# Performance work log

Measured on AMD Instinct MI355X. Metric: run time of the kernel, lower is better.

The kernel has to match this reference:

```python
import jax, jax.numpy as jnp
import numpy as np

EMBED_DIM = 1024
NUM_HEADS = 16
HEAD_DIM = EMBED_DIM // NUM_HEADS


def setup_inputs() -> dict:
    key = jax.random.key(0)
    ks = jax.random.split(key, 10)
    B, S, D = 4, 2048, EMBED_DIM
    s = 1.0 / np.sqrt(D)
    return {
        "x": jax.random.normal(ks[0], (B, S, D), dtype=jnp.float32),
        "Wq": jax.random.normal(ks[1], (D, D), dtype=jnp.float32) * s,
        "bq": jnp.zeros((D,), dtype=jnp.float32),
        "Wk": jax.random.normal(ks[2], (D, D), dtype=jnp.float32) * s,
        "bk": jnp.zeros((D,), dtype=jnp.float32),
        "Wv": jax.random.normal(ks[3], (D, D), dtype=jnp.float32) * s,
        "bv": jnp.zeros((D,), dtype=jnp.float32),
        "Wo": jax.random.normal(ks[4], (D, D), dtype=jnp.float32) * s,
        "bo": jnp.zeros((D,), dtype=jnp.float32),
        "ln_w": jnp.ones((D,), dtype=jnp.float32),
        "ln_b": jnp.zeros((D,), dtype=jnp.float32),
    }


def _layernorm(x, w, b, eps=1e-5):
    mu = jnp.mean(x, axis=-1, keepdims=True)
    var = jnp.mean(jnp.square(x - mu), axis=-1, keepdims=True)
    return (x - mu) * jax.lax.rsqrt(var + eps) * w + b


def reference(x, Wq, bq, Wk, bk, Wv, bv, Wo, bo, ln_w, ln_b):
    B, S, D = x.shape
    H, hd = NUM_HEADS, HEAD_DIM
    # projections (torch Linear: x @ W.T + b)
    q = (x @ Wq.T + bq).reshape(B, S, H, hd).transpose(0, 2, 1, 3)  # [B,H,S,hd]
    k = (x @ Wk.T + bk).reshape(B, S, H, hd).transpose(0, 2, 1, 3)
    v = (x @ Wv.T + bv).reshape(B, S, H, hd).transpose(0, 2, 1, 3)
    scores = jnp.einsum("bhqd,bhkd->bhqk", q, k) / np.sqrt(hd)
    attn = jax.nn.softmax(scores, axis=-1)
    out = jnp.einsum("bhqk,bhkd->bhqd", attn, v)
    out = out.transpose(0, 2, 1, 3).reshape(B, S, D)
    out = out @ Wo.T + bo
    return _layernorm(out, ln_w, ln_b)
```

## Files before the change

kernel.cpp:

```cpp
#include <hip/hip_runtime.h>
#include <hip/hip_bf16.h>
#include <math.h>

typedef unsigned short u16;
typedef unsigned int   u32;
typedef short bf16x8 __attribute__((ext_vector_type(8)));
typedef float f32x4  __attribute__((ext_vector_type(4)));
typedef float f32x16 __attribute__((ext_vector_type(16)));
typedef u32   u32x4  __attribute__((ext_vector_type(4)));

#define B_   4
#define S_   2048
#define D_   1024
#define H_   16
#define HD_  64
#define M_   (B_*S_)

static __device__ __forceinline__ u16 f2bf(float f) {
  __hip_bfloat16 h = __float2bfloat16(f);
  return *reinterpret_cast<u16*>(&h);
}
static __device__ __forceinline__ u32 pack_bf(float lo, float hi) {
  return (u32)f2bf(lo) | ((u32)f2bf(hi) << 16);
}
static __device__ __forceinline__ u32 pack_bf_trunc(float lo, float hi) {
  return __builtin_amdgcn_perm(__float_as_uint(hi), __float_as_uint(lo), 0x07060302u);
}
static __device__ __forceinline__ f32x16 zero16() {
  f32x16 z;
#pragma unroll
  for (int i = 0; i < 16; ++i) z[i] = 0.f;
  return z;
}

typedef __attribute__((address_space(1))) const u32* gas_t;
typedef __attribute__((address_space(3))) u32* las_t;
static __device__ __forceinline__ void g2l16(const void* g, void* l) {
  __builtin_amdgcn_global_load_lds((gas_t)g, (las_t)l, 16, 0, 0);
}

__global__ __launch_bounds__(256) void cast_all(const float* __restrict__ x,
                                                const float* __restrict__ Wq,
                                                const float* __restrict__ Wk,
                                                const float* __restrict__ Wv,
                                                const float* __restrict__ Wo,
                                                u16* __restrict__ xb,
                                                u16* __restrict__ Wqb,
                                                u16* __restrict__ Wkb,
                                                u16* __restrict__ Wvb,
                                                u16* __restrict__ Wob) {
  int bid = blockIdx.x;
  const float* src;
  u16* dst;
  int off;
  if (bid < 8192) {
    src = x; dst = xb; off = bid;
  } else {
    int t = bid - 8192;
    int w = t >> 10;
    off   = t & 1023;
    src = w == 0 ? Wq : w == 1 ? Wk : w == 2 ? Wv : Wo;
    dst = w == 0 ? Wqb : w == 1 ? Wkb : w == 2 ? Wvb : Wob;
  }
  int i = (off * 256 + threadIdx.x) * 4;
  float4 v = *reinterpret_cast<const float4*>(src + i);
  uint2 o;
  o.x = pack_bf(v.x, v.y);
  o.y = pack_bf(v.z, v.w);
  *reinterpret_cast<uint2*>(dst + i) = o;
}

__global__ __launch_bounds__(256) void gemm_qkv(const u16* __restrict__ A,
                                                const u16* __restrict__ Wq,
                                                const u16* __restrict__ Wk,
                                                const u16* __restrict__ Wv,
                                                const float* __restrict__ bq,
                                                const float* __restrict__ bk,
                                                const float* __restrict__ bv,
                                                u16* __restrict__ Qo,
                                                u16* __restrict__ Ko,
                                                u16* __restrict__ Vo) {
  const int tid  = threadIdx.x;
  const int lane = tid & 63;
  const int wave = tid >> 6;
  const int m16  = lane & 15;
  const int quad = lane >> 4;
  const int wm   = wave & 1;
  const int wn   = wave >> 1;
  const int which = blockIdx.x % 3;
  const int m0   = (blockIdx.x / 3) * 128;
  const int n0   = blockIdx.y * 128;

  const u16* W = which == 0 ? Wq : which == 1 ? Wk : Wv;
  const float* bias = which == 0 ? bq : which == 1 ? bk : bv;

  __shared__ __align__(16) u16 As[128 * 32];
  __shared__ __align__(16) u16 Bs[128 * 32];

  f32x4 acc[4][4];
#pragma unroll
  for (int i = 0; i < 4; ++i)
#pragma unroll
    for (int j = 0; j < 4; ++j) acc[i][j] = (f32x4){0.f, 0.f, 0.f, 0.f};

  for (int k0 = 0; k0 < 1024; k0 += 32) {
#pragma unroll
    for (int i = 0; i < 2; ++i) {
      int e0  = i * 256 + (wave << 6);
      int e   = e0 + lane;
      int row = e >> 2;
      int c8  = (e & 3) * 8;
      g2l16(&A[(size_t)(m0 + row) * 1024 + k0 + c8], &As[e0 * 8]);
      g2l16(&W[(size_t)(n0 + row) * 1024 + k0 + c8], &Bs[e0 * 8]);
    }
    __syncthreads();

    bf16x8 af[4], bfr[4];
#pragma unroll
    for (int mt = 0; mt < 4; ++mt)
      af[mt] = *reinterpret_cast<const bf16x8*>(&As[(wm * 64 + mt * 16 + m16) * 32 + quad * 8]);
#pragma unroll
    for (int nt = 0; nt < 4; ++nt)
      bfr[nt] = *reinterpret_cast<const bf16x8*>(&Bs[(wn * 64 + nt * 16 + m16) * 32 + quad * 8]);

#pragma unroll
    for (int mt = 0; mt < 4; ++mt)
#pragma unroll
      for (int nt = 0; nt < 4; ++nt)
        acc[mt][nt] = __builtin_amdgcn_mfma_f32_16x16x32_bf16(af[mt], bfr[nt], acc[mt][nt], 0, 0, 0);
    __syncthreads();
  }

  const float scale = which == 0 ? 0.125f * 1.44269504f : 1.0f;
  u16* ob = which == 0 ? Qo : which == 1 ? Ko : Vo;
#pragma unroll
  for (int mt = 0; mt < 4; ++mt) {
#pragma unroll
    for (int nt = 0; nt < 4; ++nt) {
      int col = n0 + wn * 64 + nt * 16 + m16;
      float bi = bias[col];
      int row0 = m0 + wm * 64 + mt * 16 + quad * 4;
      int b = row0 >> 11, s = row0 & 2047;
      int h = col >> 6,  d = col & 63;
      float v[4];
#pragma unroll
      for (int r = 0; r < 4; ++r) v[r] = (acc[mt][nt][r] + bi) * scale;
      if (which < 2) {
#pragma unroll
        for (int r = 0; r < 4; ++r)
          ob[(size_t)((b * H_ + h) * S_ + s + r) * HD_ + d] = f2bf(v[r]);
      } else {
        uint2 w;
        w.x = pack_bf(v[0], v[1]);
        w.y = pack_bf(v[2], v[3]);
        *reinterpret_cast<uint2*>(&ob[(size_t)((b * H_ + h) * HD_ + d) * S_ + s]) = w;
      }
    }
  }
}

__global__ __launch_bounds__(256) void gemm_bt(const u16* __restrict__ A,
                                               const u16* __restrict__ W,
                                               const float* __restrict__ bias,
                                               float* __restrict__ out) {
  const int tid  = threadIdx.x;
  const int lane = tid & 63;
  const int wave = tid >> 6;
  const int m16  = lane & 15;
  const int quad = lane >> 4;
  const int wm   = wave & 1;
  const int wn   = wave >> 1;
  const int m0   = blockIdx.x * 128;
  const int n0   = blockIdx.y * 128;

  __shared__ __align__(16) u16 As[128 * 32];
  __shared__ __align__(16) u16 Bs[128 * 32];

  f32x4 acc[4][4];
#pragma unroll
  for (int i = 0; i < 4; ++i)
#pragma unroll
    for (int j = 0; j < 4; ++j) acc[i][j] = (f32x4){0.f, 0.f, 0.f, 0.f};

  for (int k0 = 0; k0 < 1024; k0 += 32) {
#pragma unroll
    for (int i = 0; i < 2; ++i) {
      int e0  = i * 256 + (wave << 6);
      int e   = e0 + lane;
      int row = e >> 2;
      int c8  = (e & 3) * 8;
      g2l16(&A[(size_t)(m0 + row) * 1024 + k0 + c8], &As[e0 * 8]);
      g2l16(&W[(size_t)(n0 + row) * 1024 + k0 + c8], &Bs[e0 * 8]);
    }
    __syncthreads();

    bf16x8 af[4], bfr[4];
#pragma unroll
    for (int mt = 0; mt < 4; ++mt)
      af[mt] = *reinterpret_cast<const bf16x8*>(&As[(wm * 64 + mt * 16 + m16) * 32 + quad * 8]);
#pragma unroll
    for (int nt = 0; nt < 4; ++nt)
      bfr[nt] = *reinterpret_cast<const bf16x8*>(&Bs[(wn * 64 + nt * 16 + m16) * 32 + quad * 8]);

#pragma unroll
    for (int mt = 0; mt < 4; ++mt)
#pragma unroll
      for (int nt = 0; nt < 4; ++nt)
        acc[mt][nt] = __builtin_amdgcn_mfma_f32_16x16x32_bf16(af[mt], bfr[nt], acc[mt][nt], 0, 0, 0);
    __syncthreads();
  }

#pragma unroll
  for (int mt = 0; mt < 4; ++mt) {
#pragma unroll
    for (int nt = 0; nt < 4; ++nt) {
      int col = n0 + wn * 64 + nt * 16 + m16;
      float bi = bias[col];
#pragma unroll
      for (int r = 0; r < 4; ++r) {
        int row = m0 + wm * 64 + mt * 16 + quad * 4 + r;
        out[(size_t)row * 1024 + col] = acc[mt][nt][r] + bi;
      }
    }
  }
}

__global__ __launch_bounds__(256, 4) void attn_kernel(const u16* __restrict__ Q,
                                                      const u16* __restrict__ K,
                                                      const u16* __restrict__ Vt,
                                                      u16* __restrict__ out) {
  const int tid  = threadIdx.x;
  const int lane = tid & 63;
  const int wave = tid >> 6;
  const int r32  = lane & 31;
  const int h32  = lane >> 5;
  const int bh   = blockIdx.y;
  const int q0   = blockIdx.x * 128 + wave * 32;

  __shared__ __align__(16) u16 Ks[64 * 72];
  __shared__ __align__(16) u16 Vs[64 * 72];

  const u16* kbase = K  + (size_t)bh * S_ * HD_;
  const u16* vbase = Vt + (size_t)bh * HD_ * S_;
  const int e  = tid;
  const int e2 = tid + 256;
  const int row_a = e >> 3,  c8_a = (e & 7) * 8;
  const int row_b = e2 >> 3, c8_b = (e2 & 7) * 8;

  bf16x8 qf[4];
  {
    const u16* qbase = Q + (size_t)(bh * S_ + q0 + r32) * HD_ + h32 * 8;
#pragma unroll
    for (int dc = 0; dc < 4; ++dc)
      qf[dc] = *reinterpret_cast<const bf16x8*>(qbase + dc * 16);
  }

  f32x16 acc[2];
#pragma unroll
  for (int dt = 0; dt < 2; ++dt) acc[dt] = zero16();
  float lsum = 0.f;

  uint4 kr0 = *reinterpret_cast<const uint4*>(&kbase[(size_t)row_a * HD_ + c8_a]);
  uint4 kr1 = *reinterpret_cast<const uint4*>(&kbase[(size_t)row_b * HD_ + c8_b]);
  uint4 vr0 = *reinterpret_cast<const uint4*>(&vbase[(size_t)row_a * S_ + c8_a]);
  uint4 vr1 = *reinterpret_cast<const uint4*>(&vbase[(size_t)row_b * S_ + c8_b]);

  const int NT = S_ / 64;
  for (int kt = 0; kt < NT; ++kt) {
    *reinterpret_cast<uint4*>(&Ks[row_a * 72 + c8_a]) = kr0;
    *reinterpret_cast<uint4*>(&Ks[row_b * 72 + c8_b]) = kr1;
    *reinterpret_cast<uint4*>(&Vs[row_a * 72 + c8_a]) = vr0;
    *reinterpret_cast<uint4*>(&Vs[row_b * 72 + c8_b]) = vr1;
    __syncthreads();

    {
      const int kn = (kt + 1 < NT ? kt + 1 : kt) * 64;
      kr0 = *reinterpret_cast<const uint4*>(&kbase[(size_t)(kn + row_a) * HD_ + c8_a]);
      kr1 = *reinterpret_cast<const uint4*>(&kbase[(size_t)(kn + row_b) * HD_ + c8_b]);
      vr0 = *reinterpret_cast<const uint4*>(&vbase[(size_t)row_a * S_ + kn + c8_a]);
      vr1 = *reinterpret_cast<const uint4*>(&vbase[(size_t)row_b * S_ + kn + c8_b]);
    }

    f32x16 sc[2];
#pragma unroll
    for (int nt = 0; nt < 2; ++nt) {
      sc[nt] = zero16();
#pragma unroll
      for (int dc = 0; dc < 4; ++dc) {
        bf16x8 kf = *reinterpret_cast<const bf16x8*>(&Ks[(nt * 32 + r32) * 72 + dc * 16 + h32 * 8]);
        sc[nt] = __builtin_amdgcn_mfma_f32_32x32x16_bf16(kf, qf[dc], sc[nt], 0, 0, 0);
      }
    }

    u32 pk[2][8];
    float ps = 0.f;
#pragma unroll
    for (int nt = 0; nt < 2; ++nt)
#pragma unroll
      for (int i = 0; i < 8; ++i) {
        float p0 = __builtin_amdgcn_exp2f(sc[nt][2 * i]);
        float p1 = __builtin_amdgcn_exp2f(sc[nt][2 * i + 1]);
        ps += p0 + p1;
        pk[nt][i] = pack_bf_trunc(p0, p1);
      }
    lsum += ps;

#pragma unroll
    for (int nt = 0; nt < 2; ++nt) {
#pragma unroll
      for (int kc2 = 0; kc2 < 2; ++kc2) {
        u32 s0 = h32 ? pk[nt][4 * kc2 + 0] : pk[nt][4 * kc2 + 2];
        u32 s1 = h32 ? pk[nt][4 * kc2 + 1] : pk[nt][4 * kc2 + 3];
        u32 x0 = (u32)__shfl_xor((int)s0, 32);
        u32 x1 = (u32)__shfl_xor((int)s1, 32);
        u32x4 bw;
        bw[0] = h32 ? x0 : pk[nt][4 * kc2 + 0];
        bw[1] = h32 ? x1 : pk[nt][4 * kc2 + 1];
        bw[2] = h32 ? pk[nt][4 * kc2 + 2] : x0;
        bw[3] = h32 ? pk[nt][4 * kc2 + 3] : x1;
        bf16x8 pfrag = *reinterpret_cast<bf16x8*>(&bw);
        const int kc = nt * 2 + kc2;
#pragma unroll
        for (int dt = 0; dt < 2; ++dt) {
          bf16x8 vf = *reinterpret_cast<const bf16x8*>(&Vs[(dt * 32 + r32) * 72 + kc * 16 + h32 * 8]);
          acc[dt] = __builtin_amdgcn_mfma_f32_32x32x16_bf16(vf, pfrag, acc[dt], 0, 0, 0);
        }
      }
    }
    __syncthreads();
  }

  const int b = bh >> 4, hh = bh & 15;
  float lt  = lsum + __shfl_xor(lsum, 32);
  float inv = 1.f / lt;
  int srow = q0 + r32;
  u16* orow = out + (size_t)(b * S_ + srow) * D_ + hh * HD_;
#pragma unroll
  for (int dt = 0; dt < 2; ++dt) {
#pragma unroll
    for (int g = 0; g < 4; ++g) {
      uint2 w;
      w.x = pack_bf(acc[dt][4 * g + 0] * inv, acc[dt][4 * g + 1] * inv);
      w.y = pack_bf(acc[dt][4 * g + 2] * inv, acc[dt][4 * g + 3] * inv);
      *reinterpret_cast<uint2*>(orow + dt * 32 + 8 * g + 4 * h32) = w;
    }
  }
}

__global__ __launch_bounds__(256) void ln_kernel(const float* __restrict__ X,
                                                 const float* __restrict__ w,
                                                 const float* __restrict__ b,
                                                 float* __restrict__ out) {
  const int row = blockIdx.x;
  const int tid = threadIdx.x;
  const float* x = X + (size_t)row * 1024;
  float vals[4];
  float s = 0.f, s2 = 0.f;
#pragma unroll
  for (int i = 0; i < 4; ++i) {
    float v = x[tid + i * 256];
    vals[i] = v;
    s += v;
    s2 += v * v;
  }
#pragma unroll
  for (int off = 32; off; off >>= 1) {
    s  += __shfl_xor(s, off);
    s2 += __shfl_xor(s2, off);
  }
  __shared__ float a1[4], a2[4];
  if ((tid & 63) == 0) { a1[tid >> 6] = s; a2[tid >> 6] = s2; }
  __syncthreads();
  s  = a1[0] + a1[1] + a1[2] + a1[3];
  s2 = a2[0] + a2[1] + a2[2] + a2[3];
  float mu  = s * (1.f / 1024.f);
  float var = s2 * (1.f / 1024.f) - mu * mu;
  float inv = rsqrtf(var + 1e-5f);
#pragma unroll
  for (int i = 0; i < 4; ++i) {
    int c = tid + i * 256;
    out[(size_t)row * 1024 + c] = (vals[i] - mu) * inv * w[c] + b[c];
  }
}

extern "C" void kernel_launch(void* const* d_in, const int* in_sizes, int n_in,
                              void* d_out, int out_size, void* d_ws, size_t ws_size,
                              hipStream_t stream) {
  const float* x   = (const float*)d_in[0];
  const float* Wq  = (const float*)d_in[1];
  const float* bq  = (const float*)d_in[2];
  const float* Wk  = (const float*)d_in[3];
  const float* bk  = (const float*)d_in[4];
  const float* Wv  = (const float*)d_in[5];
  const float* bv  = (const float*)d_in[6];
  const float* Wo  = (const float*)d_in[7];
  const float* bo  = (const float*)d_in[8];
  const float* lnw = (const float*)d_in[9];
  const float* lnb = (const float*)d_in[10];

  const size_t MB = 1024ull * 1024ull;
  char* ws = (char*)d_ws;
  u16* xb  = (u16*)(ws + 0);
  u16* Qb  = (u16*)(ws + 16 * MB);
  u16* Kb  = (u16*)(ws + 32 * MB);
  u16* Vtb = (u16*)(ws + 48 * MB);
  u16* Wqb = (u16*)(ws + 64 * MB);
  u16* Wkb = (u16*)(ws + 66 * MB);
  u16* Wvb = (u16*)(ws + 68 * MB);
  u16* Wob = (u16*)(ws + 70 * MB);
  float* Of = (float*)(ws + 16 * MB);

  cast_all<<<8192 + 4096, 256, 0, stream>>>(x, Wq, Wk, Wv, Wo, xb, Wqb, Wkb, Wvb, Wob);

  gemm_qkv<<<dim3((M_ / 128) * 3, D_ / 128), 256, 0, stream>>>(
      xb, Wqb, Wkb, Wvb, bq, bk, bv, Qb, Kb, Vtb);

  attn_kernel<<<dim3(S_ / 128, B_ * H_), 256, 0, stream>>>(Qb, Kb, Vtb, xb);

  gemm_bt<<<dim3(M_ / 128, D_ / 128), 256, 0, stream>>>(xb, Wob, bo, Of);

  ln_kernel<<<M_, 256, 0, stream>>>(Of, lnw, lnb, (float*)d_out);
}
```

Baseline: 305.2 us.

## Double-buffer K/V tiles, drop trailing barrier, use permlane32 swap and setprio

The attention kernel now double-buffers its K and V shared-memory tiles, which lets it remove the second __syncthreads per iteration. The P-fragment exchange between half-waves uses permlane32_swap instead of two shfl_xor plus selects. The MFMA sections are wrapped in s_setprio to raise wave priority, and the row-sum accumulation is split into two chains. The cost is doubled LDS per block, which could affect occupancy under the 4-blocks launch bound.

```diff
diff --git a/kernel.cpp b/kernel.cpp
--- a/kernel.cpp
+++ b/kernel.cpp
@@ -8,6 +8,7 @@
 typedef float f32x4  __attribute__((ext_vector_type(4)));
 typedef float f32x16 __attribute__((ext_vector_type(16)));
 typedef u32   u32x4  __attribute__((ext_vector_type(4)));
+typedef u32   u32x2  __attribute__((ext_vector_type(2)));
 
 #define B_   4
 #define S_   2048
@@ -237,8 +238,8 @@
   const int bh   = blockIdx.y;
   const int q0   = blockIdx.x * 128 + wave * 32;
 
-  __shared__ __align__(16) u16 Ks[64 * 72];
-  __shared__ __align__(16) u16 Vs[64 * 72];
+  __shared__ __align__(16) u16 Ks[2][64 * 72];
+  __shared__ __align__(16) u16 Vs[2][64 * 72];
 
   const u16* kbase = K  + (size_t)bh * S_ * HD_;
   const u16* vbase = Vt + (size_t)bh * HD_ * S_;
@@ -267,10 +268,12 @@
 
   const int NT = S_ / 64;
   for (int kt = 0; kt < NT; ++kt) {
-    *reinterpret_cast<uint4*>(&Ks[row_a * 72 + c8_a]) = kr0;
-    *reinterpret_cast<uint4*>(&Ks[row_b * 72 + c8_b]) = kr1;
-    *reinterpret_cast<uint4*>(&Vs[row_a * 72 + c8_a]) = vr0;
-    *reinterpret_cast<uint4*>(&Vs[row_b * 72 + c8_b]) = vr1;
+    u16* ks = Ks[kt & 1];
+    u16* vs = Vs[kt & 1];
+    *reinterpret_cast<uint4*>(&ks[row_a * 72 + c8_a]) = kr0;
+    *reinterpret_cast<uint4*>(&ks[row_b * 72 + c8_b]) = kr1;
+    *reinterpret_cast<uint4*>(&vs[row_a * 72 + c8_a]) = vr0;
+    *reinterpret_cast<uint4*>(&vs[row_b * 72 + c8_b]) = vr1;
     __syncthreads();
 
     {
@@ -282,52 +285,54 @@
     }
 
     f32x16 sc[2];
+    __builtin_amdgcn_s_setprio(1);
 #pragma unroll
     for (int nt = 0; nt < 2; ++nt) {
       sc[nt] = zero16();
 #pragma unroll
       for (int dc = 0; dc < 4; ++dc) {
-        bf16x8 kf = *reinterpret_cast<const bf16x8*>(&Ks[(nt * 32 + r32) * 72 + dc * 16 + h32 * 8]);
+        bf16x8 kf = *reinterpret_cast<const bf16x8*>(&ks[(nt * 32 + r32) * 72 + dc * 16 + h32 * 8]);
         sc[nt] = __builtin_amdgcn_mfma_f32_32x32x16_bf16(kf, qf[dc], sc[nt], 0, 0, 0);
       }
     }
+    __builtin_amdgcn_s_setprio(0);
 
     u32 pk[2][8];
-    float ps = 0.f;
+    float ps0 = 0.f, ps1 = 0.f;
 #pragma unroll
     for (int nt = 0; nt < 2; ++nt)
 #pragma unroll
       for (int i = 0; i < 8; ++i) {
         float p0 = __builtin_amdgcn_exp2f(sc[nt][2 * i]);
         float p1 = __builtin_amdgcn_exp2f(sc[nt][2 * i + 1]);
-        ps += p0 + p1;
+        ps0 += p0;
+        ps1 += p1;
         pk[nt][i] = pack_bf_trunc(p0, p1);
       }
-    lsum += ps;
-
+    lsum += ps0 + ps1;
+
+    __builtin_amdgcn_s_setprio(1);
 #pragma unroll
     for (int nt = 0; nt < 2; ++nt) {
 #pragma unroll
       for (int kc2 = 0; kc2 < 2; ++kc2) {
-        u32 s0 = h32 ? pk[nt][4 * kc2 + 0] : pk[nt][4 * kc2 + 2];
-        u32 s1 = h32 ? pk[nt][4 * kc2 + 1] : pk[nt][4 * kc2 + 3];
-        u32 x0 = (u32)__shfl_xor((int)s0, 32);
-        u32 x1 = (u32)__shfl_xor((int)s1, 32);
+        u32x2 r0 = __builtin_amdgcn_permlane32_swap(pk[nt][4 * kc2 + 0], pk[nt][4 * kc2 + 2], false, false);
+        u32x2 r1 = __builtin_amdgcn_permlane32_swap(pk[nt][4 * kc2 + 1], pk[nt][4 * kc2 + 3], false, false);
         u32x4 bw;
-        bw[0] = h32 ? x0 : pk[nt][4 * kc2 + 0];
-        bw[1] = h32 ? x1 : pk[nt][4 * kc2 + 1];
-        bw[2] = h32 ? pk[nt][4 * kc2 + 2] : x0;
-        bw[3] = h32 ? pk[nt][4 * kc2 + 3] : x1;
+        bw[0] = r0[0];
+        bw[1] = r1[0];
+        bw[2] = r0[1];
+        bw[3] = r1[1];
         bf16x8 pfrag = *reinterpret_cast<bf16x8*>(&bw);
         const int kc = nt * 2 + kc2;
 #pragma unroll
         for (int dt = 0; dt < 2; ++dt) {
-          bf16x8 vf = *reinterpret_cast<const bf16x8*>(&Vs[(dt * 32 + r32) * 72 + kc * 16 + h32 * 8]);
+          bf16x8 vf = *reinterpret_cast<const bf16x8*>(&vs[(dt * 32 + r32) * 72 + kc * 16 + h32 * 8]);
           acc[dt] = __builtin_amdgcn_mfma_f32_32x32x16_bf16(vf, pfrag, acc[dt], 0, 0, 0);
         }
       }
     }
-    __syncthreads();
+    __builtin_amdgcn_s_setprio(0);
   }
 
   const int b = bh >> 4, hh = bh & 15;
```

Result: no change. 304.5 us (-0.2%).
